# Kernel optimization log

Hardware: AMD Instinct MI355X
Metric: run time of the kernel (lower is better)

## Reference

```python
import jax, jax.numpy as jnp
import numpy as np

D_MODEL = 2048
N_HEADS = 16
D_K = D_MODEL // N_HEADS


def setup_inputs() -> dict:
    key = jax.random.key(0)
    ks = jax.random.split(key, 9)
    s = 1.0 / np.sqrt(D_MODEL)
    def lin(k):
        kw, kb = jax.random.split(k)
        W = jax.random.uniform(kw, (D_MODEL, D_MODEL), jnp.float32, -s, s)
        b = jax.random.uniform(kb, (D_MODEL,), jnp.float32, -s, s)
        return W, b
    Wq, bq = lin(ks[0])
    Wk, bk = lin(ks[1])
    Wv, bv = lin(ks[2])
    Wo, bo = lin(ks[3])
    x = jax.random.normal(ks[4], (2, 2048, D_MODEL), jnp.float32)
    return {"x": x, "Wq": Wq, "bq": bq, "Wk": Wk, "bk": bk,
            "Wv": Wv, "bv": bv, "Wo": Wo, "bo": bo}


def _mha(x, Wq, bq, Wk, bk, Wv, bv, Wo, bo):
    B, S, _ = x.shape
    # Linear projections (torch Linear: x @ W.T + b), split into heads: b s (h d) -> b h s d
    def proj(W, b):
        y = jnp.einsum('bsm,nm->bsn', x, W) + b
        return y.reshape(B, S, N_HEADS, D_K).transpose(0, 2, 1, 3)
    q = proj(Wq, bq)
    k = proj(Wk, bk)
    v = proj(Wv, bv)
    scores = jnp.einsum('bhsd,bhtd->bhst', q, k) / jnp.sqrt(jnp.float32(D_K))
    causal = jnp.triu(jnp.ones((S, S), bool), k=1)  # True above diagonal -> masked
    scores = jnp.where(causal[None, None], -jnp.inf, scores)
    attn = jax.nn.softmax(scores, axis=-1)  # dropout p=0 (eval)
    out = jnp.einsum('bhst,bhtd->bhsd', attn, v)
    out = out.transpose(0, 2, 1, 3).reshape(B, S, D_MODEL)
    return jnp.einsum('bsm,nm->bsn', out, Wo) + bo


def reference(x, Wq, bq, Wk, bk, Wv, bv, Wo, bo):
    return _mha(x, Wq, bq, Wk, bk, Wv, bv, Wo, bo)
```

## Files before the change

kernel.cpp:

```cpp
#include <hip/hip_runtime.h>

typedef unsigned short u16;
typedef __attribute__((ext_vector_type(8))) short bf16x8;
typedef __attribute__((ext_vector_type(4))) float f32x4;
typedef __attribute__((ext_vector_type(4))) unsigned short u16x4;

__device__ __forceinline__ u16 f2bf(float f) {
  union { float f; unsigned u; } v; v.f = f;
  return (u16)((v.u + 0x7FFFu + ((v.u >> 16) & 1u)) >> 16);
}

__device__ __forceinline__ void gload16(const u16* g, u16* l) {
  __builtin_amdgcn_global_load_lds((const __attribute__((address_space(1))) void*)g,
                                   (__attribute__((address_space(3))) void*)l, 16, 0, 0);
}

__global__ __launch_bounds__(256) void k_f2bf5(
    const float* __restrict__ i0, const float* __restrict__ i1, const float* __restrict__ i2,
    const float* __restrict__ i3, const float* __restrict__ i4,
    u16* o0, u16* o1, u16* o2, u16* o3, u16* o4, int n4x, int n4w) {
  const int seg = blockIdx.y;
  const float* in = (seg == 0) ? i0 : (seg == 1) ? i1 : (seg == 2) ? i2 : (seg == 3) ? i3 : i4;
  u16* out = (seg == 0) ? o0 : (seg == 1) ? o1 : (seg == 2) ? o2 : (seg == 3) ? o3 : o4;
  const int n4 = (seg == 0) ? n4x : n4w;
  int i = blockIdx.x * 256 + threadIdx.x;
  const int stride = gridDim.x * 256;
  for (; i < n4; i += stride) {
    const float4 v = ((const float4*)in)[i];
    u16x4 o;
    o.x = f2bf(v.x); o.y = f2bf(v.y); o.z = f2bf(v.z); o.w = f2bf(v.w);
    ((u16x4*)out)[i] = o;
  }
}

#define STAGE_P0(AN, BN_, kofs) do { _Pragma("unroll") \
  for (int i = 0; i < 2; ++i) { \
    gload16(A  + (row0 + aRow[i]) * 2048L + (kofs) + aCol[i], &(AN)[aDst[i]]); \
    gload16(Bt + (col0 + brLo[i]) * 2048L + (kofs) + bcB[i], &(BN_)[bDstLo[i]]); } } while (0)

#define STAGE_P1(BN_, kofs) do { _Pragma("unroll") \
  for (int i = 0; i < 2; ++i) \
    gload16(Bt + (col0 + brLo[i] + 32) * 2048L + (kofs) + bcB[i], &(BN_)[bDstLo[i] + 2048]); } while (0)

#define MMpair(nbase) do { _Pragma("unroll") \
  for (int mi = 0; mi < 4; ++mi) { _Pragma("unroll") \
    for (int nn = 0; nn < 2; ++nn) { \
      acc[mi][(nbase) + nn] = __builtin_amdgcn_mfma_f32_16x16x32_bf16( \
          a[mi][0], b[nn][0], acc[mi][(nbase) + nn], 0, 0, 0); \
      acc[mi][(nbase) + nn] = __builtin_amdgcn_mfma_f32_16x16x32_bf16( \
          a[mi][1], b[nn][1], acc[mi][(nbase) + nn], 0, 0, 0); } } } while (0)

#define TILE(AS, BS, AN, BN_, tn, full) do { \
  _Pragma("unroll") for (int mi = 0; mi < 4; ++mi) { \
    a[mi][0] = *(const bf16x8*)&(AS)[aBase + mi * 1024 + pc0]; \
    a[mi][1] = *(const bf16x8*)&(AS)[aBase + mi * 1024 + pc1]; } \
  _Pragma("unroll") for (int nn = 0; nn < 2; ++nn) { \
    b[nn][0] = *(const bf16x8*)&(BS)[bBase + nn * 1024 + pc0]; \
    b[nn][1] = *(const bf16x8*)&(BS)[bBase + nn * 1024 + pc1]; } \
  if (full) { STAGE_P0(AN, BN_, (long)(tn) << 6); \
    asm volatile("s_waitcnt vmcnt(4)" ::: "memory"); \
  } else { asm volatile("s_waitcnt vmcnt(0)" ::: "memory"); } \
  __builtin_amdgcn_s_barrier(); \
  asm volatile("s_waitcnt lgkmcnt(0)" ::: "memory"); \
  __builtin_amdgcn_sched_barrier(0); \
  __builtin_amdgcn_s_setprio(1); MMpair(0); __builtin_amdgcn_s_setprio(0); \
  __builtin_amdgcn_s_barrier(); \
  _Pragma("unroll") for (int nn = 0; nn < 2; ++nn) { \
    b[nn][0] = *(const bf16x8*)&(BS)[bBase + (2 + nn) * 1024 + pc0]; \
    b[nn][1] = *(const bf16x8*)&(BS)[bBase + (2 + nn) * 1024 + pc1]; } \
  if (full) { STAGE_P1(BN_, (long)(tn) << 6); \
    asm volatile("s_waitcnt vmcnt(2)" ::: "memory"); \
  } else { asm volatile("s_waitcnt vmcnt(0)" ::: "memory"); } \
  __builtin_amdgcn_s_barrier(); \
  asm volatile("s_waitcnt lgkmcnt(0)" ::: "memory"); \
  __builtin_amdgcn_sched_barrier(0); \
  __builtin_amdgcn_s_setprio(1); MMpair(2); __builtin_amdgcn_s_setprio(0); \
  __builtin_amdgcn_s_barrier(); \
} while (0)

template <int OUT_F32>
__global__ __launch_bounds__(512, 2) void k_gemm256(
    const u16* __restrict__ A, const u16* __restrict__ Bt,
    const float* __restrict__ b0, const float* __restrict__ b1, const float* __restrict__ b2,
    u16* __restrict__ C0, u16* __restrict__ C1, u16* __restrict__ C2,
    float* __restrict__ Cf, int NBM)
{
  __shared__ alignas(16) u16 A0s[8192], B0s[16384], A1s[8192], B1s[16384];

  const int tid = threadIdx.x;
  const int lane = tid & 63, wid = tid >> 6;
  const int fr = lane & 15, fg = lane >> 4;
  const int wr = wid >> 2, wc = wid & 3;

  const int nblk = gridDim.x;
  const int q = nblk >> 3, r = nblk & 7;
  const int xcd = blockIdx.x & 7, lid = blockIdx.x >> 3;
  const int wgid = (xcd < r ? xcd * (q + 1) : r * (q + 1) + (xcd - r) * q) + lid;
  const int mb = wgid % NBM, nb = wgid / NBM;
  const long row0 = (long)mb * 128;
  const long col0 = (long)nb * 256;

  int aRow[2], aCol[2], brLo[2], bcB[2], aDst[2], bDstLo[2];
#pragma unroll
  for (int i = 0; i < 2; ++i) {
    const int g = (wid * 2 + i) * 64 + lane;
    aRow[i] = g >> 3;
    aCol[i] = ((g & 7) ^ (aRow[i] & 7)) << 3;
    aDst[i] = g * 8;
    const int stripe = g >> 8, rowin = (g >> 3) & 31;
    brLo[i] = stripe * 64 + rowin;
    bcB[i] = ((g & 7) ^ (brLo[i] & 7)) << 3;
    bDstLo[i] = stripe * 4096 + (g & 255) * 8;
  }

  const int sw = fr & 7;
  const int aBase = (wr * 64 + fr) * 64;
  const int bBase = (wc * 64 + fr) * 64;
  const int pc0 = (fg ^ sw) << 3;
  const int pc1 = ((4 + fg) ^ sw) << 3;

  f32x4 acc[4][4] = {};
  bf16x8 a[4][2], b[2][2];

  STAGE_P0(A0s, B0s, 0);
  STAGE_P1(B0s, 0);
  asm volatile("s_waitcnt vmcnt(0)" ::: "memory");
  __builtin_amdgcn_s_barrier();

#pragma unroll 1
  for (int t = 0; t < 30; t += 2) {
    TILE(A0s, B0s, A1s, B1s, t + 1, 1);
    TILE(A1s, B1s, A0s, B0s, t + 2, 1);
  }
  TILE(A0s, B0s, A1s, B1s, 31, 1);
  TILE(A1s, B1s, A0s, B0s, 32, 0);

  const int seg = (int)(col0 >> 11);
  const long colL = col0 & 2047;
  const float* bp = (seg == 0) ? b0 : (seg == 1) ? b1 : b2;
  u16* Cb = (seg == 0) ? C0 : (seg == 1) ? C1 : C2;
#pragma unroll
  for (int n = 0; n < 4; ++n) {
    const long cN = colL + wc * 64 + n * 16 + fr;
    const float bv = bp[cN];
#pragma unroll
    for (int mi = 0; mi < 4; ++mi) {
      const long rM = row0 + wr * 64 + mi * 16 + fg * 4;
#pragma unroll
      for (int reg = 0; reg < 4; ++reg) {
        const float v = acc[mi][n][reg] + bv;
        if (OUT_F32) Cf[(rM + reg) * 2048 + cN] = v;
        else         Cb[(rM + reg) * 2048 + cN] = f2bf(v);
      }
    }
  }
}

__global__ __launch_bounds__(256) void k_transpose_v(const u16* __restrict__ V,
                                                     u16* __restrict__ Vt) {
  __shared__ u16 t[64][68];
  const int bh = blockIdx.z;
  const long s0 = (long)blockIdx.x * 64;
  const long d0 = (long)blockIdx.y * 64;
  const int tid = threadIdx.x;
  const long rowbase = (long)(bh >> 4) * 2048;
  const int hcol = (bh & 15) * 128;
#pragma unroll
  for (int i = 0; i < 4; ++i) {
    const int v = tid + i * 256;
    const int r = v >> 4, c4 = (v & 15) << 2;
    const u16x4 val = *(const u16x4*)&V[(rowbase + s0 + r) * 2048 + hcol + d0 + c4];
    *(u16x4*)&t[r][c4] = val;
  }
  __syncthreads();
#pragma unroll
  for (int i = 0; i < 4; ++i) {
    const int v = tid + i * 256;
    const int dr = v >> 4, s4 = (v & 15) << 2;
    u16x4 o;
    o.x = t[s4 + 0][dr]; o.y = t[s4 + 1][dr]; o.z = t[s4 + 2][dr]; o.w = t[s4 + 3][dr];
    *(u16x4*)&Vt[((long)bh * 128 + d0 + dr) * 2048 + s0 + s4] = o;
  }
}

__global__ __launch_bounds__(512) void k_flash_attn(
    const u16* __restrict__ Q, const u16* __restrict__ K, const u16* __restrict__ Vt,
    u16* __restrict__ O)
{
  __shared__ alignas(16) u16 Kt[2][8192];
  __shared__ alignas(16) u16 Vtt[2][8192];
  __shared__ alignas(16) u16 Plds[8][16][72];

  const int tid = threadIdx.x;
  const int lane = tid & 63, wid = tid >> 6;
  const int fr = lane & 15, fg = lane >> 4;

  const int L = blockIdx.x;
  const int bh = (L & 7) * 4 + ((L >> 3) & 3);
  const int bx = L >> 5;

  const long rowbase = (long)(bh >> 4) * 2048;
  const int hcol = (bh & 15) * 128;
  const u16* Kg = K + rowbase * 2048 + hcol;
  const u16* Vg = Vt + (long)bh * 128 * 2048;
  const float scale2 = 0.08838834764831845f * 1.44269504089f;

  int kR[2], kC[2], vR[2], vC[2];
#pragma unroll
  for (int i = 0; i < 2; ++i) {
    const int chunk = (wid * 2 + i) * 64 + lane;
    kR[i] = chunk >> 4;
    kC[i] = ((chunk & 15) ^ (kR[i] & 7)) << 3;
    vR[i] = chunk >> 3;
    vC[i] = ((chunk & 7) ^ (vR[i] & 7)) << 3;
  }

  const int sw = fr & 7;
  int kbase[4], vbase[2];
#pragma unroll
  for (int c = 0; c < 4; ++c) kbase[c] = fr * 128 + (((c * 4 + fg) ^ sw) << 3);
#pragma unroll
  for (int kc = 0; kc < 2; ++kc) vbase[kc] = fr * 64 + (((kc * 4 + fg) ^ sw) << 3);

  for (int pass = 0; pass < 2; ++pass) {
    const int qblk = pass ? (15 - bx) : bx;
    const int n = 2 * (qblk + 1);
    const int q_lo = qblk * 128 + wid * 16;

    bf16x8 qf[4];
#pragma unroll
    for (int c = 0; c < 4; ++c)
      qf[c] = *(const bf16x8*)&Q[(rowbase + q_lo + fr) * 2048 + hcol + c * 32 + fg * 8];

    f32x4 oacc[8] = {};
    float m_run[4], l_run[4];
#pragma unroll
    for (int r = 0; r < 4; ++r) { m_run[r] = -1e30f; l_run[r] = 0.0f; }

#pragma unroll
    for (int i = 0; i < 2; ++i) {
      gload16(Kg + (long)kR[i] * 2048 + kC[i], &Kt[0][(wid * 2 + i) * 512]);
      gload16(Vg + (long)vR[i] * 2048 + vC[i], &Vtt[0][(wid * 2 + i) * 512]);
    }

    int cur = 0;
    for (int j = 0; j < n; ++j) {
      if (j + 1 < n) {
        const long kv = (long)(j + 1) * 64;
#pragma unroll
        for (int i = 0; i < 2; ++i) {
          gload16(Kg + (kv + kR[i]) * 2048 + kC[i], &Kt[cur ^ 1][(wid * 2 + i) * 512]);
          gload16(Vg + (long)vR[i] * 2048 + kv + vC[i], &Vtt[cur ^ 1][(wid * 2 + i) * 512]);
        }
        asm volatile("s_waitcnt vmcnt(4)" ::: "memory");
      } else {
        asm volatile("s_waitcnt vmcnt(0)" ::: "memory");
      }
      __builtin_amdgcn_s_barrier();
      __builtin_amdgcn_sched_barrier(0);

      const int kvlo = j * 64;
      const bool skip = (kvlo >= q_lo + 16);
      if (!skip) {
        const bool needmask = (kvlo + 63 > q_lo);

        f32x4 st[4] = {};
        const u16* kt = Kt[cur];
#pragma unroll
        for (int t = 0; t < 4; ++t)
#pragma unroll
          for (int c = 0; c < 4; ++c) {
            const bf16x8 kf = *(const bf16x8*)&kt[kbase[c] + t * 2048];
            st[t] = __builtin_amdgcn_mfma_f32_16x16x32_bf16(qf[c], kf, st[t], 0, 0, 0);
          }

        float pmax[4] = {-1e30f, -1e30f, -1e30f, -1e30f};
        if (needmask) {
#pragma unroll
          for (int t = 0; t < 4; ++t) {
            const int kg = kvlo + t * 16 + fr;
#pragma unroll
            for (int r = 0; r < 4; ++r) {
              const int qg = q_lo + fg * 4 + r;
              const float v = (kg <= qg) ? st[t][r] * scale2 : -1e30f;
              st[t][r] = v;
              pmax[r] = fmaxf(pmax[r], v);
            }
          }
        } else {
#pragma unroll
          for (int t = 0; t < 4; ++t)
#pragma unroll
            for (int r = 0; r < 4; ++r) {
              const float v = st[t][r] * scale2;
              st[t][r] = v;
              pmax[r] = fmaxf(pmax[r], v);
            }
        }
#pragma unroll
        for (int d = 1; d < 16; d <<= 1)
#pragma unroll
          for (int r = 0; r < 4; ++r) pmax[r] = fmaxf(pmax[r], __shfl_xor(pmax[r], d));

        const int ok = (pmax[0] <= m_run[0] + 8.f) & (pmax[1] <= m_run[1] + 8.f) &
                       (pmax[2] <= m_run[2] + 8.f) & (pmax[3] <= m_run[3] + 8.f);
        if (!__all(ok)) {
#pragma unroll
          for (int r = 0; r < 4; ++r) {
            const float nm = fmaxf(m_run[r], pmax[r]);
            const float al = exp2f(m_run[r] - nm);
            l_run[r] *= al;
            m_run[r] = nm;
#pragma unroll
            for (int dt = 0; dt < 8; ++dt) oacc[dt][r] *= al;
          }
        }

        float lsum[4] = {0.f, 0.f, 0.f, 0.f};
#pragma unroll
        for (int t = 0; t < 4; ++t)
#pragma unroll
          for (int r = 0; r < 4; ++r) {
            const float p = exp2f(st[t][r] - m_run[r]);
            st[t][r] = p;
            lsum[r] += p;
          }
#pragma unroll
        for (int d = 1; d < 16; d <<= 1)
#pragma unroll
          for (int r = 0; r < 4; ++r) lsum[r] += __shfl_xor(lsum[r], d);
#pragma unroll
        for (int r = 0; r < 4; ++r) l_run[r] += lsum[r];

#pragma unroll
        for (int t = 0; t < 4; ++t)
#pragma unroll
          for (int r = 0; r < 4; ++r)
            Plds[wid][fg * 4 + r][t * 16 + fr] = f2bf(st[t][r]);
        asm volatile("s_waitcnt lgkmcnt(0)" ::: "memory");
        __builtin_amdgcn_sched_barrier(0);

        const u16* vt = Vtt[cur];
#pragma unroll
        for (int kc = 0; kc < 2; ++kc) {
          const bf16x8 pf = *(const bf16x8*)&Plds[wid][fr][kc * 32 + fg * 8];
#pragma unroll
          for (int dt = 0; dt < 8; ++dt) {
            const bf16x8 vf = *(const bf16x8*)&vt[vbase[kc] + dt * 1024];
            oacc[dt] = __builtin_amdgcn_mfma_f32_16x16x32_bf16(pf, vf, oacc[dt], 0, 0, 0);
          }
        }
      }

      asm volatile("" ::: "memory");
      __builtin_amdgcn_s_barrier();
      cur ^= 1;
    }

    float inv[4];
#pragma unroll
    for (int r = 0; r < 4; ++r) inv[r] = 1.0f / l_run[r];
#pragma unroll
    for (int dt = 0; dt < 8; ++dt)
#pragma unroll
      for (int r = 0; r < 4; ++r)
        O[(rowbase + q_lo + fg * 4 + r) * 2048 + hcol + dt * 16 + fr] = f2bf(oacc[dt][r] * inv[r]);
  }
}

extern "C" void kernel_launch(void* const* d_in, const int* in_sizes, int n_in,
                              void* d_out, int out_size, void* d_ws, size_t ws_size,
                              hipStream_t stream) {
  const float* x  = (const float*)d_in[0];
  const float* Wq = (const float*)d_in[1];
  const float* bq = (const float*)d_in[2];
  const float* Wk = (const float*)d_in[3];
  const float* bk = (const float*)d_in[4];
  const float* Wv = (const float*)d_in[5];
  const float* bv = (const float*)d_in[6];
  const float* Wo = (const float*)d_in[7];
  const float* bo = (const float*)d_in[8];
  float* out = (float*)d_out;

  char* ws = (char*)d_ws;
  const size_t SZ_X = 16777216;
  const size_t SZ_W = 8388608;
  u16* xb  = (u16*)(ws);
  u16* wqb = (u16*)(ws + SZ_X);
  u16* wkb = (u16*)(ws + SZ_X + 1 * SZ_W);
  u16* wvb = (u16*)(ws + SZ_X + 2 * SZ_W);
  u16* wob = (u16*)(ws + SZ_X + 3 * SZ_W);
  u16* Qb  = (u16*)(ws + 1 * SZ_X + 4 * SZ_W);
  u16* Kb  = (u16*)(ws + 2 * SZ_X + 4 * SZ_W);
  u16* Vb  = (u16*)(ws + 3 * SZ_X + 4 * SZ_W);
  u16* Vtb = (u16*)(ws + 4 * SZ_X + 4 * SZ_W);
  u16* Ob  = Vb;

  k_f2bf5<<<dim3(1024, 5), 256, 0, stream>>>(x, Wq, Wk, Wv, Wo,
                                             xb, wqb, wkb, wvb, wob,
                                             8388608 / 4, 4194304 / 4);

  k_gemm256<0><<<768, 512, 0, stream>>>(xb, wqb, bq, bk, bv, Qb, Kb, Vb, nullptr, 32);

  k_transpose_v<<<dim3(32, 2, 32), 256, 0, stream>>>(Vb, Vtb);

  k_flash_attn<<<256, 512, 0, stream>>>(Qb, Kb, Vtb, Ob);

  k_gemm256<1><<<256, 512, 0, stream>>>(Ob, wob, bo, bo, bo, nullptr, nullptr, nullptr, out, 32);
}
```

Baseline: 296.5 us.

## Software-pipeline LDS fragment reads in GEMM with register double-buffering

Result: faster. 289.9 us (-2.2%).

```diff
diff --git a/kernel.cpp b/kernel.cpp
--- a/kernel.cpp
+++ b/kernel.cpp
@@ -33,59 +33,83 @@
   }
 }
 
-#define STAGE_P0(AN, BN_, kofs) do { _Pragma("unroll") \
+#define STAGE_V1(AN, BN_, kofs) do { _Pragma("unroll") \
   for (int i = 0; i < 2; ++i) { \
     gload16(A  + (row0 + aRow[i]) * 2048L + (kofs) + aCol[i], &(AN)[aDst[i]]); \
     gload16(Bt + (col0 + brLo[i]) * 2048L + (kofs) + bcB[i], &(BN_)[bDstLo[i]]); } } while (0)
 
-#define STAGE_P1(BN_, kofs) do { _Pragma("unroll") \
+#define STAGE_V2(BN_, kofs) do { _Pragma("unroll") \
   for (int i = 0; i < 2; ++i) \
     gload16(Bt + (col0 + brLo[i] + 32) * 2048L + (kofs) + bcB[i], &(BN_)[bDstLo[i] + 2048]); } while (0)
 
-#define MMpair(nbase) do { _Pragma("unroll") \
+#define RD_AB0(AS, BS, AR, B0R) do { _Pragma("unroll") \
+  for (int mi = 0; mi < 4; ++mi) { \
+    AR[mi][0] = *(const bf16x8*)&(AS)[aBase + mi * 1024 + pc0]; \
+    AR[mi][1] = *(const bf16x8*)&(AS)[aBase + mi * 1024 + pc1]; } \
+  _Pragma("unroll") for (int nn = 0; nn < 2; ++nn) { \
+    B0R[nn][0] = *(const bf16x8*)&(BS)[bBase + nn * 1024 + pc0]; \
+    B0R[nn][1] = *(const bf16x8*)&(BS)[bBase + nn * 1024 + pc1]; } } while (0)
+
+#define RD_B1(BS) do { _Pragma("unroll") \
+  for (int nn = 0; nn < 2; ++nn) { \
+    b1[nn][0] = *(const bf16x8*)&(BS)[bBase + (2 + nn) * 1024 + pc0]; \
+    b1[nn][1] = *(const bf16x8*)&(BS)[bBase + (2 + nn) * 1024 + pc1]; } } while (0)
+
+#define MMQ(AR, BR, nb) do { _Pragma("unroll") \
   for (int mi = 0; mi < 4; ++mi) { _Pragma("unroll") \
     for (int nn = 0; nn < 2; ++nn) { \
-      acc[mi][(nbase) + nn] = __builtin_amdgcn_mfma_f32_16x16x32_bf16( \
-          a[mi][0], b[nn][0], acc[mi][(nbase) + nn], 0, 0, 0); \
-      acc[mi][(nbase) + nn] = __builtin_amdgcn_mfma_f32_16x16x32_bf16( \
-          a[mi][1], b[nn][1], acc[mi][(nbase) + nn], 0, 0, 0); } } } while (0)
-
-#define TILE(AS, BS, AN, BN_, tn, full) do { \
-  _Pragma("unroll") for (int mi = 0; mi < 4; ++mi) { \
-    a[mi][0] = *(const bf16x8*)&(AS)[aBase + mi * 1024 + pc0]; \
-    a[mi][1] = *(const bf16x8*)&(AS)[aBase + mi * 1024 + pc1]; } \
-  _Pragma("unroll") for (int nn = 0; nn < 2; ++nn) { \
-    b[nn][0] = *(const bf16x8*)&(BS)[bBase + nn * 1024 + pc0]; \
-    b[nn][1] = *(const bf16x8*)&(BS)[bBase + nn * 1024 + pc1]; } \
-  if (full) { STAGE_P0(AN, BN_, (long)(tn) << 6); \
-    asm volatile("s_waitcnt vmcnt(4)" ::: "memory"); \
-  } else { asm volatile("s_waitcnt vmcnt(0)" ::: "memory"); } \
+      acc[mi][(nb) + nn] = __builtin_amdgcn_mfma_f32_16x16x32_bf16( \
+          AR[mi][0], BR[nn][0], acc[mi][(nb) + nn], 0, 0, 0); \
+      acc[mi][(nb) + nn] = __builtin_amdgcn_mfma_f32_16x16x32_bf16( \
+          AR[mi][1], BR[nn][1], acc[mi][(nb) + nn], 0, 0, 0); } } } while (0)
+
+#define PH1_F(BS, AN, BN_, AR, B0R, tn) do { \
+  STAGE_V1(AN, BN_, (long)(tn) << 6); \
+  asm volatile("s_waitcnt vmcnt(4)" ::: "memory"); \
+  __builtin_amdgcn_s_barrier(); \
+  asm volatile("" ::: "memory"); \
+  RD_B1(BS); \
+  asm volatile("s_waitcnt lgkmcnt(4)" ::: "memory"); \
+  __builtin_amdgcn_sched_barrier(0); \
+  __builtin_amdgcn_s_setprio(1); MMQ(AR, B0R, 0); __builtin_amdgcn_s_setprio(0); \
+} while (0)
+
+#define PH2_F(ANX, BNX, ARc, ARn, B0Rn, tn) do { \
+  STAGE_V2(BNX, (long)(tn) << 6); \
+  asm volatile("s_waitcnt vmcnt(2)" ::: "memory"); \
+  __builtin_amdgcn_s_barrier(); \
+  asm volatile("" ::: "memory"); \
+  RD_AB0(ANX, BNX, ARn, B0Rn); \
+  asm volatile("s_waitcnt lgkmcnt(12)" ::: "memory"); \
+  __builtin_amdgcn_sched_barrier(0); \
+  __builtin_amdgcn_s_setprio(1); MMQ(ARc, b1, 2); __builtin_amdgcn_s_setprio(0); \
+} while (0)
+
+#define PH1_L(BS, AR, B0R) do { \
+  asm volatile("s_waitcnt vmcnt(0)" ::: "memory"); \
+  __builtin_amdgcn_s_barrier(); \
+  asm volatile("" ::: "memory"); \
+  RD_B1(BS); \
+  asm volatile("s_waitcnt lgkmcnt(4)" ::: "memory"); \
+  __builtin_amdgcn_sched_barrier(0); \
+  __builtin_amdgcn_s_setprio(1); MMQ(AR, B0R, 0); __builtin_amdgcn_s_setprio(0); \
+} while (0)
+
+#define PH2_L(ARc) do { \
   __builtin_amdgcn_s_barrier(); \
   asm volatile("s_waitcnt lgkmcnt(0)" ::: "memory"); \
   __builtin_amdgcn_sched_barrier(0); \
-  __builtin_amdgcn_s_setprio(1); MMpair(0); __builtin_amdgcn_s_setprio(0); \
-  __builtin_amdgcn_s_barrier(); \
-  _Pragma("unroll") for (int nn = 0; nn < 2; ++nn) { \
-    b[nn][0] = *(const bf16x8*)&(BS)[bBase + (2 + nn) * 1024 + pc0]; \
-    b[nn][1] = *(const bf16x8*)&(BS)[bBase + (2 + nn) * 1024 + pc1]; } \
-  if (full) { STAGE_P1(BN_, (long)(tn) << 6); \
-    asm volatile("s_waitcnt vmcnt(2)" ::: "memory"); \
-  } else { asm volatile("s_waitcnt vmcnt(0)" ::: "memory"); } \
-  __builtin_amdgcn_s_barrier(); \
-  asm volatile("s_waitcnt lgkmcnt(0)" ::: "memory"); \
-  __builtin_amdgcn_sched_barrier(0); \
-  __builtin_amdgcn_s_setprio(1); MMpair(2); __builtin_amdgcn_s_setprio(0); \
-  __builtin_amdgcn_s_barrier(); \
+  __builtin_amdgcn_s_setprio(1); MMQ(ARc, b1, 2); __builtin_amdgcn_s_setprio(0); \
 } while (0)
 
 template <int OUT_F32>
-__global__ __launch_bounds__(512, 2) void k_gemm256(
+__global__ __launch_bounds__(512, 2) void k_gemm128(
     const u16* __restrict__ A, const u16* __restrict__ Bt,
-    const float* __restrict__ b0, const float* __restrict__ b1, const float* __restrict__ b2,
+    const float* __restrict__ b0, const float* __restrict__ b1_, const float* __restrict__ b2,
     u16* __restrict__ C0, u16* __restrict__ C1, u16* __restrict__ C2,
     float* __restrict__ Cf, int NBM)
 {
-  __shared__ alignas(16) u16 A0s[8192], B0s[16384], A1s[8192], B1s[16384];
+  __shared__ alignas(16) u16 As0[8192], Bs0[16384], As1[8192], Bs1[16384];
 
   const int tid = threadIdx.x;
   const int lane = tid & 63, wid = tid >> 6;
@@ -120,24 +144,30 @@
   const int pc1 = ((4 + fg) ^ sw) << 3;
 
   f32x4 acc[4][4] = {};
-  bf16x8 a[4][2], b[2][2];
-
-  STAGE_P0(A0s, B0s, 0);
-  STAGE_P1(B0s, 0);
+  bf16x8 aA[4][2], aB[4][2], b0A[2][2], b0B[2][2], b1[2][2];
+
+  STAGE_V1(As0, Bs0, 0);
+  STAGE_V2(Bs0, 0);
   asm volatile("s_waitcnt vmcnt(0)" ::: "memory");
   __builtin_amdgcn_s_barrier();
+  asm volatile("" ::: "memory");
+  RD_AB0(As0, Bs0, aA, b0A);
 
 #pragma unroll 1
   for (int t = 0; t < 30; t += 2) {
-    TILE(A0s, B0s, A1s, B1s, t + 1, 1);
-    TILE(A1s, B1s, A0s, B0s, t + 2, 1);
-  }
-  TILE(A0s, B0s, A1s, B1s, 31, 1);
-  TILE(A1s, B1s, A0s, B0s, 32, 0);
+    PH1_F(Bs0, As1, Bs1, aA, b0A, t + 1);
+    PH2_F(As1, Bs1, aA, aB, b0B, t + 1);
+    PH1_F(Bs1, As0, Bs0, aB, b0B, t + 2);
+    PH2_F(As0, Bs0, aB, aA, b0A, t + 2);
+  }
+  PH1_F(Bs0, As1, Bs1, aA, b0A, 31);
+  PH2_F(As1, Bs1, aA, aB, b0B, 31);
+  PH1_L(Bs1, aB, b0B);
+  PH2_L(aB);
 
   const int seg = (int)(col0 >> 11);
   const long colL = col0 & 2047;
-  const float* bp = (seg == 0) ? b0 : (seg == 1) ? b1 : b2;
+  const float* bp = (seg == 0) ? b0 : (seg == 1) ? b1_ : b2;
   u16* Cb = (seg == 0) ? C0 : (seg == 1) ? C1 : C2;
 #pragma unroll
   for (int n = 0; n < 4; ++n) {
@@ -400,11 +430,11 @@
                                              xb, wqb, wkb, wvb, wob,
                                              8388608 / 4, 4194304 / 4);
 
-  k_gemm256<0><<<768, 512, 0, stream>>>(xb, wqb, bq, bk, bv, Qb, Kb, Vb, nullptr, 32);
+  k_gemm128<0><<<768, 512, 0, stream>>>(xb, wqb, bq, bk, bv, Qb, Kb, Vb, nullptr, 32);
 
   k_transpose_v<<<dim3(32, 2, 32), 256, 0, stream>>>(Vb, Vtb);
 
   k_flash_attn<<<256, 512, 0, stream>>>(Qb, Kb, Vtb, Ob);
 
-  k_gemm256<1><<<256, 512, 0, stream>>>(Ob, wob, bo, bo, bo, nullptr, nullptr, nullptr, out, 32);
-}
+  k_gemm128<1><<<256, 512, 0, stream>>>(Ob, wob, bo, bo, bo, nullptr, nullptr, nullptr, out, 32);
+}
```
